# Performance work log

Hardware: AMD Instinct MI355X
Metric: run time of the kernel (lower is better)

The kernel has to match this reference:

```python
import jax, jax.numpy as jnp
import numpy as np

N_NODES = 50000
N_EDGES = 800000
N_GRAPHS = 64
EMB_DIM = 24
N_KERNELS = 2
M_DIM = 64
FOURIER = 4
POS_DIM = 3
EDGE_IN = 2 * FOURIER + 1 + 2 * EMB_DIM  # 57
MLP_DIM = 256
N_OUT = 4
FFNN_IN = EMB_DIM * (N_KERNELS + 1)  # 72


def _lin(key, fan_in, fan_out, stack=None):
    # xavier-uniform weight, zero bias (matches weights_init)
    lim = (6.0 / (fan_in + fan_out)) ** 0.5
    shp = ((stack,) if stack else ()) + (fan_in, fan_out)
    w = jax.random.uniform(key, shp, minval=-lim, maxval=lim, dtype=jnp.float32)
    b = jnp.zeros(((stack,) if stack else ()) + (fan_out,), jnp.float32)
    return w, b


def setup_inputs() -> dict:
    key = jax.random.key(0)
    ks = jax.random.split(key, 20)
    z = jax.random.randint(ks[0], (N_NODES,), 0, 22)
    pos = jax.random.normal(ks[1], (N_NODES, POS_DIM), jnp.float32)
    edge_index = jax.random.randint(ks[2], (2, N_EDGES), 0, N_NODES)
    batch_idx = jnp.sort(jax.random.randint(ks[3], (N_NODES,), 0, N_GRAPHS))
    lim_e = (6.0 / (22 + EMB_DIM)) ** 0.5
    emb_table = jax.random.uniform(ks[4], (22, EMB_DIM), minval=-lim_e, maxval=lim_e, dtype=jnp.float32)
    emb_w, emb_b = _lin(ks[5], EMB_DIM, EMB_DIM)
    # EGNN kernel params, stacked over N_KERNELS
    ew1, eb1 = _lin(ks[6], EDGE_IN, EDGE_IN * 2, N_KERNELS)
    ew2, eb2 = _lin(ks[7], EDGE_IN * 2, M_DIM, N_KERNELS)
    cw1, cb1 = _lin(ks[8], M_DIM, M_DIM * 4, N_KERNELS)
    cw2, cb2 = _lin(ks[9], M_DIM * 4, 1, N_KERNELS)
    nw1, nb1 = _lin(ks[10], EMB_DIM + M_DIM, EMB_DIM * 2, N_KERNELS)
    nw2, nb2 = _lin(ks[11], EMB_DIM * 2, EMB_DIM, N_KERNELS)
    # ffnn: Linear(72,256), Linear(256,256), Linear(256,256), Linear(256,4)
    f0w, f0b = _lin(ks[12], FFNN_IN, MLP_DIM)
    f1w, f1b = _lin(ks[13], MLP_DIM, MLP_DIM)
    f2w, f2b = _lin(ks[14], MLP_DIM, MLP_DIM)
    fow, fob = _lin(ks[15], MLP_DIM, N_OUT)
    return dict(z=z, pos=pos, edge_index=edge_index, batch_idx=batch_idx,
                emb_table=emb_table, emb_w=emb_w, emb_b=emb_b,
                ew1=ew1, eb1=eb1, ew2=ew2, eb2=eb2,
                cw1=cw1, cb1=cb1, cw2=cw2, cb2=cb2,
                nw1=nw1, nb1=nb1, nw2=nw2, nb2=nb2,
                f0w=f0w, f0b=f0b, f1w=f1w, f1b=f1b, f2w=f2w, f2b=f2b,
                fow=fow, fob=fob)


def _egnn_layer(feats, coors, src, dst, ew1, eb1, ew2, eb2, cw1, cb1, cw2, cb2, nw1, nb1, nw2, nb2):
    # EGNN_sparse (PyG flow source_to_target: i=dst=edge_index[1], j=src=edge_index[0])
    rel = coors[src] - coors[dst]                       # [E,3]
    d = jnp.sum(rel * rel, axis=-1, keepdims=True)      # [E,1] squared distance
    scales = 2.0 ** jnp.arange(FOURIER, dtype=feats.dtype)
    ds = d / scales                                     # [E,4]
    edge_feat = jnp.concatenate([jnp.sin(ds), jnp.cos(ds), d], axis=-1)  # [E,9]
    e_in = jnp.concatenate([feats[dst], feats[src], edge_feat], axis=-1)  # [E,57]
    m_ij = jax.nn.silu(jax.nn.silu(e_in @ ew1 + eb1) @ ew2 + eb2)         # [E,64]
    coor_w = jax.nn.silu(m_ij @ cw1 + cb1) @ cw2 + cb2                    # [E,1]
    coors_out = coors + jax.ops.segment_sum(coor_w * rel, dst, num_segments=N_NODES)
    m_i = jax.ops.segment_sum(m_ij, dst, num_segments=N_NODES)            # [N,64]
    h = jax.nn.silu(jnp.concatenate([feats, m_i], axis=-1) @ nw1 + nb1)
    feats_out = feats + (h @ nw2 + nb2)
    return feats_out, coors_out


def reference(z, pos, edge_index, batch_idx, emb_table, emb_w, emb_b,
              ew1, eb1, ew2, eb2, cw1, cb1, cw2, cb2, nw1, nb1, nw2, nb2,
              f0w, f0b, f1w, f1b, f2w, f2b, fow, fob):
    src, dst = edge_index[0], edge_index[1]
    feats = emb_table[z] @ emb_w + emb_b
    coors = pos
    flist = [feats]
    for k in range(N_KERNELS):
        feats, coors = _egnn_layer(feats, coors, src, dst,
                                   ew1[k], eb1[k], ew2[k], eb2[k],
                                   cw1[k], cb1[k], cw2[k], cb2[k],
                                   nw1[k], nb1[k], nw2[k], nb2[k])
        flist.append(feats)
    x = jax.nn.silu(jnp.concatenate(flist, axis=-1))     # [N,72]
    x = jax.nn.silu(x @ f0w + f0b)
    x = jax.nn.silu(x @ f1w + f1b)
    x = jax.nn.silu(x @ f2w + f2b)                       # [N,256]
    cnt = jax.ops.segment_sum(jnp.ones((x.shape[0],), x.dtype), batch_idx, num_segments=N_GRAPHS)
    pooled = jax.ops.segment_sum(x, batch_idx, num_segments=N_GRAPHS) / jnp.maximum(cnt, 1.0)[:, None]
    return jax.nn.sigmoid(pooled @ fow + fob)            # [B,4]
```

## Files before the change

### kernel.cpp

```cpp
#include <hip/hip_runtime.h>
#include <hip/hip_bf16.h>

#define N_NODES  50000
#define N_EDGES  800000
#define N_GRAPHS 64
#define EMB      24
#define MDIM     64
#define EDGE_IN  57
#define EH       114
#define CH       256
#define NIN      88
#define NH       48
#define MLP      256
#define ETILE    128
#define NTILE    64

typedef __bf16 bf16_t;
typedef __bf16 bf16x8 __attribute__((ext_vector_type(8)));
typedef __bf16 bf16x4 __attribute__((ext_vector_type(4)));
typedef float  f32x4  __attribute__((ext_vector_type(4)));

__device__ __forceinline__ float siluf(float x) {
    return x * __builtin_amdgcn_rcpf(1.0f + __expf(-x));
}

__device__ __forceinline__ f32x4 silu4(f32x4 x) {
    f32x4 t = x * (-1.44269504088896341f);
    f32x4 e;
    e[0] = __builtin_amdgcn_exp2f(t[0]);
    e[1] = __builtin_amdgcn_exp2f(t[1]);
    e[2] = __builtin_amdgcn_exp2f(t[2]);
    e[3] = __builtin_amdgcn_exp2f(t[3]);
    f32x4 den = e + 1.0f;
    f32x4 r;
    r[0] = __builtin_amdgcn_rcpf(den[0]);
    r[1] = __builtin_amdgcn_rcpf(den[1]);
    r[2] = __builtin_amdgcn_rcpf(den[2]);
    r[3] = __builtin_amdgcn_rcpf(den[3]);
    return x * r;
}

__device__ __forceinline__ bf16x8 cat44(bf16x4 a, bf16x4 b) {
    bf16x8 r;
    r[0]=a[0]; r[1]=a[1]; r[2]=a[2]; r[3]=a[3];
    r[4]=b[0]; r[5]=b[1]; r[6]=b[2]; r[7]=b[3];
    return r;
}

__global__ void embed_kernel(const int* __restrict__ z, const float* __restrict__ table,
                             const float* __restrict__ w, const float* __restrict__ b,
                             const int* __restrict__ batch, float* __restrict__ f0,
                             bf16_t* __restrict__ fb0, float* __restrict__ cnt)
{
    int n = blockIdx.x * blockDim.x + threadIdx.x;
    if (n >= N_NODES) return;
    float r[EMB];
    const float4* tr = reinterpret_cast<const float4*>(table + z[n] * EMB);
    #pragma unroll
    for (int q = 0; q < 6; q++) {
        float4 v = tr[q];
        r[q*4] = v.x; r[q*4+1] = v.y; r[q*4+2] = v.z; r[q*4+3] = v.w;
    }
    float o[EMB];
    #pragma unroll
    for (int j = 0; j < EMB; j++) o[j] = b[j];
    #pragma unroll
    for (int i = 0; i < EMB; i++) {
        #pragma unroll
        for (int j = 0; j < EMB; j++) o[j] = fmaf(r[i], w[i*EMB + j], o[j]);
    }
    float4* dst = reinterpret_cast<float4*>(f0 + (size_t)n * EMB);
    #pragma unroll
    for (int q = 0; q < 6; q++) dst[q] = make_float4(o[q*4], o[q*4+1], o[q*4+2], o[q*4+3]);
    bf16x8* bdst = reinterpret_cast<bf16x8*>(fb0 + (size_t)n * EMB);
    #pragma unroll
    for (int q = 0; q < 3; q++) {
        bf16x8 pk;
        #pragma unroll
        for (int j = 0; j < 8; j++) pk[j] = (bf16_t)o[q*8 + j];
        bdst[q] = pk;
    }
    atomicAdd(&cnt[batch[n]], 1.0f);
}

#define PK_W1   (128*64)
#define PK_W2   (64*128)
#define PK_CW   (256*64)
#define PK_F0   (256*128)
#define PK_FM   (256*256)
#define PK_TOT  (2*PK_W1 + 2*PK_W2 + PK_CW + PK_F0 + 2*PK_FM)
__global__ void pack_kernel(const float* __restrict__ ew1, const float* __restrict__ eb1,
                            const float* __restrict__ ew2, const float* __restrict__ eb2,
                            const float* __restrict__ cw1, const float* __restrict__ f0w,
                            const float* __restrict__ f1w, const float* __restrict__ f2w,
                            bf16_t* __restrict__ pw)
{
    int idx = blockIdx.x * blockDim.x + threadIdx.x;
    if (idx >= PK_TOT) return;
    float v = 0.0f;
    if (idx < 2 * PK_W1) {
        int l = idx / PK_W1, r = idx - l * PK_W1;
        int n = r >> 6, k = r & 63;
        if (n < EH && k < EDGE_IN)       v = ew1[(l * EDGE_IN + k) * EH + n];
        else if (n < EH && k == EDGE_IN) v = eb1[l * EH + n];
    } else if (idx < 2 * PK_W1 + 2 * PK_W2) {
        int r0 = idx - 2 * PK_W1;
        int l = r0 / PK_W2, r = r0 - l * PK_W2;
        int n = r >> 7, kp = r & 127;
        int ks = kp >> 5, g = (kp >> 3) & 3, j = kp & 7;
        int f = 16 * (2*ks + (j >> 2)) + 4*g + (j & 3);
        if (f < EH)       v = ew2[(l * EH + f) * MDIM + n];
        else if (f == EH) v = eb2[l * MDIM + n];
    } else if (idx < 2 * PK_W1 + 2 * PK_W2 + PK_CW) {
        int r = idx - (2 * PK_W1 + 2 * PK_W2);
        int n = r >> 6, kp = r & 63;
        int ks = kp >> 5, g = (kp >> 3) & 3, j = kp & 7;
        int f = 16 * (2*ks + (j >> 2)) + 4*g + (j & 3);
        v = cw1[f * CH + n];
    } else if (idx < 2 * PK_W1 + 2 * PK_W2 + PK_CW + PK_F0) {
        int r = idx - (2 * PK_W1 + 2 * PK_W2 + PK_CW);
        int n = r >> 7, k = r & 127;
        if (k < 72) v = f0w[k * MLP + n];
    } else {
        int r0 = idx - (2 * PK_W1 + 2 * PK_W2 + PK_CW + PK_F0);
        int l = r0 / PK_FM, r = r0 - l * PK_FM;
        int n = r >> 8, k = r & 255;
        v = (l == 0) ? f1w[k * MLP + n] : f2w[k * MLP + n];
    }
    pw[idx] = (bf16_t)v;
}

__global__ void hist_kernel(const int* __restrict__ dst, int* __restrict__ deg)
{
    int e = blockIdx.x * blockDim.x + threadIdx.x;
    if (e < N_EDGES) atomicAdd(&deg[dst[e]], 1);
}

__global__ __launch_bounds__(1024)
void scan_kernel(const int* __restrict__ deg, int* __restrict__ cursor)
{
    __shared__ int part[1024];
    int t = threadIdx.x;
    const int PER = 49;
    int base = t * PER;
    int s = 0;
    for (int i = 0; i < PER; i++) {
        int p = base + i;
        if (p < N_NODES) s += deg[p];
    }
    part[t] = s;
    __syncthreads();
    for (int off = 1; off < 1024; off <<= 1) {
        int add = (t >= off) ? part[t - off] : 0;
        __syncthreads();
        part[t] += add;
        __syncthreads();
    }
    int run = (t > 0) ? part[t - 1] : 0;
    for (int i = 0; i < PER; i++) {
        int p = base + i;
        if (p < N_NODES) { cursor[p] = run; run += deg[p]; }
    }
}

__global__ void scatter_kernel(const int* __restrict__ src, const int* __restrict__ dst,
                               int* __restrict__ cursor, int* __restrict__ srcs_s,
                               int* __restrict__ dsts_s)
{
    int e = blockIdx.x * blockDim.x + threadIdx.x;
    if (e >= N_EDGES) return;
    int d = dst[e];
    int pos = atomicAdd(&cursor[d], 1);
    srcs_s[pos] = src[e];
    dsts_s[pos] = d;
}

template<int COOR>
__global__ __launch_bounds__(256, 4)
void edge_mfma(const bf16_t* __restrict__ fb, const float* __restrict__ coors,
               const int* __restrict__ srcs_s, const int* __restrict__ dsts_s,
               const bf16_t* __restrict__ W1t, const bf16_t* __restrict__ W2t,
               const bf16_t* __restrict__ CW1t, const float* __restrict__ cb1,
               const float* __restrict__ cw2, const float* __restrict__ cb2,
               float* __restrict__ m_i, float* __restrict__ cdelta)
{
    __shared__ __align__(16) char R1raw[4 * 4096];
    __shared__ float s_rel[COOR ? ETILE * 3 : 4];
    __shared__ float s_cacc[COOR ? ETILE : 4];
    __shared__ int   s_dst[ETILE];

    const int t = threadIdx.x;
    const int w = t >> 6;
    const int l = t & 63;
    const int row0 = w * 32;
    const int ebase = blockIdx.x * ETILE;
    const int l15 = l & 15, l4 = l >> 4;
    bf16_t* slab16 = (bf16_t*)(R1raw + w * 4096);

    {
        int e_loc = t >> 1, half = t & 1;
        int e_l = e_loc & 31;
        int e = ebase + e_loc;
        int s = srcs_s[e], d = dsts_s[e];
        if (half == 0) {
            s_dst[e_loc] = d;
            const bf16x8* fp = reinterpret_cast<const bf16x8*>(fb + (size_t)d * EMB);
            #pragma unroll
            for (int g = 0; g < 3; g++)
                *(bf16x8*)&slab16[e_l*64 + (g ^ (e_l & 7))*8] = fp[g];
        } else {
            const bf16x8* fp = reinterpret_cast<const bf16x8*>(fb + (size_t)s * EMB);
            #pragma unroll
            for (int g = 0; g < 3; g++)
                *(bf16x8*)&slab16[e_l*64 + ((g + 3) ^ (e_l & 7))*8] = fp[g];
            float rx = coors[s*3+0] - coors[d*3+0];
            float ry = coors[s*3+1] - coors[d*3+1];
            float rz = coors[s*3+2] - coors[d*3+2];
            float d2 = rx*rx + ry*ry + rz*rz;
            if (COOR) { s_rel[e_loc*3+0] = rx; s_rel[e_loc*3+1] = ry; s_rel[e_loc*3+2] = rz; }
            bf16x8 p6, p7;
            p6[0]=(bf16_t)__sinf(d2);        p6[1]=(bf16_t)__sinf(d2*0.5f);
            p6[2]=(bf16_t)__sinf(d2*0.25f);  p6[3]=(bf16_t)__sinf(d2*0.125f);
            p6[4]=(bf16_t)__cosf(d2);        p6[5]=(bf16_t)__cosf(d2*0.5f);
            p6[6]=(bf16_t)__cosf(d2*0.25f);  p6[7]=(bf16_t)__cosf(d2*0.125f);
            p7[0]=(bf16_t)d2; p7[1]=(bf16_t)1.0f;
            p7[2]=(bf16_t)0.f; p7[3]=(bf16_t)0.f; p7[4]=(bf16_t)0.f;
            p7[5]=(bf16_t)0.f; p7[6]=(bf16_t)0.f; p7[7]=(bf16_t)0.f;
            *(bf16x8*)&slab16[e_l*64 + (6 ^ (e_l & 7))*8] = p6;
            *(bf16x8*)&slab16[e_l*64 + (7 ^ (e_l & 7))*8] = p7;
        }
    }

    f32x4 acc1[2][8];
    #pragma unroll
    for (int et = 0; et < 2; et++)
        #pragma unroll
        for (int ft = 0; ft < 8; ft++) acc1[et][ft] = (f32x4){0.f,0.f,0.f,0.f};
    __builtin_amdgcn_s_setprio(1);
    #pragma unroll
    for (int ks = 0; ks < 2; ks++) {
        bf16x8 bfrag[2];
        #pragma unroll
        for (int et = 0; et < 2; et++) {
            int e_l = et*16 + l15;
            bfrag[et] = *(const bf16x8*)&slab16[e_l*64 + ((ks*4 + l4) ^ (e_l & 7))*8];
        }
        #pragma unroll
        for (int ft = 0; ft < 8; ft++) {
            bf16x8 a = *(const bf16x8*)&W1t[(ft*16 + l15)*64 + (ks*4 + l4)*8];
            acc1[0][ft] = __builtin_amdgcn_mfma_f32_16x16x32_bf16(a, bfrag[0], acc1[0][ft], 0, 0, 0);
            acc1[1][ft] = __builtin_amdgcn_mfma_f32_16x16x32_bf16(a, bfrag[1], acc1[1][ft], 0, 0, 0);
        }
    }
    __builtin_amdgcn_s_setprio(0);

    bf16x4 h1b[2][8];
    #pragma unroll
    for (int et = 0; et < 2; et++)
        #pragma unroll
        for (int ft = 0; ft < 8; ft++) {
            f32x4 hv = silu4(acc1[et][ft]);
            if (ft == 7 && l4 == 0) hv[2] = 1.0f;
            bf16x4 pk;
            #pragma unroll
            for (int r4 = 0; r4 < 4; r4++) pk[r4] = (bf16_t)hv[r4];
            h1b[et][ft] = pk;
        }

    f32x4 acc2[2][4];
    #pragma unroll
    for (int et = 0; et < 2; et++)
        #pragma unroll
        for (int ft = 0; ft < 4; ft++) acc2[et][ft] = (f32x4){0.f,0.f,0.f,0.f};
    __builtin_amdgcn_s_setprio(1);
    #pragma unroll
    for (int ks = 0; ks < 4; ks++) {
        bf16x8 bfrag0 = cat44(h1b[0][2*ks], h1b[0][2*ks+1]);
        bf16x8 bfrag1 = cat44(h1b[1][2*ks], h1b[1][2*ks+1]);
        #pragma unroll
        for (int ft = 0; ft < 4; ft++) {
            bf16x8 a = *(const bf16x8*)&W2t[(ft*16 + l15)*128 + (ks*4 + l4)*8];
            acc2[0][ft] = __builtin_amdgcn_mfma_f32_16x16x32_bf16(a, bfrag0, acc2[0][ft], 0, 0, 0);
            acc2[1][ft] = __builtin_amdgcn_mfma_f32_16x16x32_bf16(a, bfrag1, acc2[1][ft], 0, 0, 0);
        }
    }
    __builtin_amdgcn_s_setprio(0);

    bf16x4 mb[2][4];
    #pragma unroll
    for (int et = 0; et < 2; et++)
        #pragma unroll
        for (int ft = 0; ft < 4; ft++) {
            int e_l = et*16 + l15;
            int f0 = ft*16 + l4*4;
            f32x4 mv = silu4(acc2[et][ft]);
            bf16x4 pk;
            #pragma unroll
            for (int r4 = 0; r4 < 4; r4++) pk[r4] = (bf16_t)mv[r4];
            mb[et][ft] = pk;
            *(bf16x4*)&slab16[e_l*64 + (((f0 >> 2) ^ (e_l & 7)) << 2)] = pk;
        }

    {
        int col = l;
        int gsw = col >> 2, cw = col & 3;
        int cur = s_dst[row0];
        float run = 0.f;
        for (int i = 0; i < 32; i++) {
            int d = s_dst[row0 + i];
            float v = (float)slab16[i*64 + ((gsw ^ (i & 7)) << 2) + cw];
            if (d != cur) { atomicAdd(&m_i[(size_t)cur*64 + col], run); run = 0.f; cur = d; }
            run += v;
        }
        atomicAdd(&m_i[(size_t)cur*64 + col], run);
    }

    if (COOR) {
        f32x4 csumv0 = (f32x4){0.f,0.f,0.f,0.f};
        f32x4 csumv1 = (f32x4){0.f,0.f,0.f,0.f};
        #pragma unroll
        for (int half = 0; half < 2; half++) {
            f32x4 acc3[2][8];
            #pragma unroll
            for (int et = 0; et < 2; et++)
                #pragma unroll
                for (int ft = 0; ft < 8; ft++) acc3[et][ft] = (f32x4){0.f,0.f,0.f,0.f};
            __builtin_amdgcn_s_setprio(1);
            #pragma unroll
            for (int ks = 0; ks < 2; ks++) {
                bf16x8 bfrag0 = cat44(mb[0][2*ks], mb[0][2*ks+1]);
                bf16x8 bfrag1 = cat44(mb[1][2*ks], mb[1][2*ks+1]);
                #pragma unroll
                for (int ft = 0; ft < 8; ft++) {
                    bf16x8 a = *(const bf16x8*)&CW1t[(half*128 + ft*16 + l15)*64 + (ks*4 + l4)*8];
                    acc3[0][ft] = __builtin_amdgcn_mfma_f32_16x16x32_bf16(a, bfrag0, acc3[0][ft], 0, 0, 0);
                    acc3[1][ft] = __builtin_amdgcn_mfma_f32_16x16x32_bf16(a, bfrag1, acc3[1][ft], 0, 0, 0);
                }
            }
            __builtin_amdgcn_s_setprio(0);
            #pragma unroll
            for (int ft = 0; ft < 8; ft++) {
                int f0 = half*128 + ft*16 + l4*4;
                f32x4 c1 = *(const f32x4*)&cb1[f0];
                f32x4 w2 = *(const f32x4*)&cw2[f0];
                csumv0 += silu4(acc3[0][ft] + c1) * w2;
                csumv1 += silu4(acc3[1][ft] + c1) * w2;
            }
        }
        float csum0 = (csumv0[0] + csumv0[1]) + (csumv0[2] + csumv0[3]);
        float csum1 = (csumv1[0] + csumv1[1]) + (csumv1[2] + csumv1[3]);
        csum0 += __shfl_xor(csum0, 16);
        csum0 += __shfl_xor(csum0, 32);
        csum1 += __shfl_xor(csum1, 16);
        csum1 += __shfl_xor(csum1, 32);
        float cb2v = cb2[0];
        if (l < 32) {
            s_cacc[row0 + l] = ((l & 16) ? csum1 : csum0) + cb2v;
        }
        if (l < 32) {
            int row = row0 + l;
            int d = s_dst[row];
            bool head = (l == 0) || (s_dst[row - 1] != d);
            if (head) {
                float ax = 0.f, ay = 0.f, az = 0.f;
                int i = l;
                do {
                    int r = row0 + i;
                    float c = s_cacc[r];
                    ax = fmaf(c, s_rel[r*3+0], ax);
                    ay = fmaf(c, s_rel[r*3+1], ay);
                    az = fmaf(c, s_rel[r*3+2], az);
                    ++i;
                } while (i < 32 && s_dst[row0 + i] == d);
                atomicAdd(&cdelta[d*3+0], ax);
                atomicAdd(&cdelta[d*3+1], ay);
                atomicAdd(&cdelta[d*3+2], az);
            }
        }
    }
}

template<int EMIT_BF16>
__global__ __launch_bounds__(256)
void node_kernel(const float* __restrict__ feats, const float* __restrict__ m_i,
                 const float* __restrict__ nw1, const float* __restrict__ nb1,
                 const float* __restrict__ nw2, const float* __restrict__ nb2,
                 float* __restrict__ fout, bf16_t* __restrict__ fbout)
{
    __shared__ float s_w1t[NH * NIN];
    __shared__ float s_b1[NH];
    __shared__ float s_w2[NH * EMB];
    __shared__ float s_b2[EMB];
    const int tid = threadIdx.x;
    for (int idx = tid; idx < NH * NIN; idx += 256) {
        int k = idx / NIN, i = idx - k * NIN;
        s_w1t[idx] = nw1[i * NH + k];
    }
    for (int idx = tid; idx < NH * EMB; idx += 256) s_w2[idx] = nw2[idx];
    if (tid < NH) s_b1[tid] = nb1[tid];
    if (tid < EMB) s_b2[tid] = nb2[tid];
    __syncthreads();

    int n = blockIdx.x * 256 + tid;
    if (n >= N_NODES) return;

    float in[NIN];
    const float4* fp = reinterpret_cast<const float4*>(feats + (size_t)n * EMB);
    #pragma unroll
    for (int q = 0; q < 6; q++) {
        float4 v = fp[q];
        in[q*4] = v.x; in[q*4+1] = v.y; in[q*4+2] = v.z; in[q*4+3] = v.w;
    }
    const float4* mp = reinterpret_cast<const float4*>(m_i + (size_t)n * MDIM);
    #pragma unroll
    for (int q = 0; q < 16; q++) {
        float4 v = mp[q];
        in[EMB+q*4] = v.x; in[EMB+q*4+1] = v.y; in[EMB+q*4+2] = v.z; in[EMB+q*4+3] = v.w;
    }
    float o[EMB];
    #pragma unroll
    for (int j = 0; j < EMB; j++) o[j] = in[j] + s_b2[j];
    for (int k = 0; k < NH; k++) {
        const float* w1 = &s_w1t[k * NIN];
        float a0 = 0.f, a1 = 0.f, a2 = 0.f, a3 = 0.f;
        #pragma unroll
        for (int i = 0; i < NIN; i += 4) {
            a0 = fmaf(in[i],   w1[i],   a0);
            a1 = fmaf(in[i+1], w1[i+1], a1);
            a2 = fmaf(in[i+2], w1[i+2], a2);
            a3 = fmaf(in[i+3], w1[i+3], a3);
        }
        float h = siluf(s_b1[k] + ((a0 + a1) + (a2 + a3)));
        const float* w2 = &s_w2[k * EMB];
        #pragma unroll
        for (int j = 0; j < EMB; j++) o[j] = fmaf(h, w2[j], o[j]);
    }
    float4* dst = reinterpret_cast<float4*>(fout + (size_t)n * EMB);
    #pragma unroll
    for (int q = 0; q < 6; q++) dst[q] = make_float4(o[q*4], o[q*4+1], o[q*4+2], o[q*4+3]);
    if (EMIT_BF16) {
        bf16x8* bdst = reinterpret_cast<bf16x8*>(fbout + (size_t)n * EMB);
        #pragma unroll
        for (int q = 0; q < 3; q++) {
            bf16x8 pk;
            #pragma unroll
            for (int j = 0; j < 8; j++) pk[j] = (bf16_t)o[q*8 + j];
            bdst[q] = pk;
        }
    }
}

__global__ void coor_kernel(const float* __restrict__ pos, const float* __restrict__ cdelta,
                            float* __restrict__ out)
{
    int i = blockIdx.x * blockDim.x + threadIdx.x;
    if (i < N_NODES * 3) out[i] = pos[i] + cdelta[i];
}

__global__ __launch_bounds__(512, 4)
void ffnn_fused(const float* __restrict__ f0, const float* __restrict__ f1,
                const float* __restrict__ f2,
                const bf16_t* __restrict__ W0p, const bf16_t* __restrict__ W1p,
                const bf16_t* __restrict__ W2p,
                const float* __restrict__ b0, const float* __restrict__ b1,
                const float* __restrict__ b2,
                const int* __restrict__ batch, float* __restrict__ pooled)
{
    __shared__ __align__(16) bf16_t sH[NTILE * 256];
    __shared__ int s_batch[NTILE];
    const int t = threadIdx.x;
    const int w = t >> 6, l = t & 63;
    const int l15 = l & 15, q = l >> 4;
    const int mt = w & 3;
    const int nh = w >> 2;
    const int mrow0 = mt * 16;
    const int n0 = blockIdx.x * NTILE;

    {
        int row = t >> 3, part = t & 7;
        int n = n0 + row;
        bool valid = n < N_NODES;
        if (part == 7) s_batch[row] = valid ? batch[n] : -1;
        #pragma unroll
        for (int gi = 0; gi < 2; gi++) {
            int g = part * 2 + gi;
            bf16x8 pk;
            #pragma unroll
            for (int j = 0; j < 8; j++) pk[j] = (bf16_t)0.f;
            if (valid && g < 9) {
                const float* sp = (g < 3) ? f0 + (size_t)n*EMB + 8*g
                                : (g < 6) ? f1 + (size_t)n*EMB + 8*(g-3)
                                          : f2 + (size_t)n*EMB + 8*(g-6);
                float4 a = ((const float4*)sp)[0], b = ((const float4*)sp)[1];
                f32x4 sa = silu4((f32x4){a.x, a.y, a.z, a.w});
                f32x4 sb = silu4((f32x4){b.x, b.y, b.z, b.w});
                pk[0]=(bf16_t)sa[0]; pk[1]=(bf16_t)sa[1]; pk[2]=(bf16_t)sa[2]; pk[3]=(bf16_t)sa[3];
                pk[4]=(bf16_t)sb[0]; pk[5]=(bf16_t)sb[1]; pk[6]=(bf16_t)sb[2]; pk[7]=(bf16_t)sb[3];
            }
            *(bf16x8*)&sH[row*128 + (g ^ (row & 7))*8] = pk;
        }
    }
    __syncthreads();

    bf16x8 a0[4];
    {
        int r = mrow0 + l15;
        #pragma unroll
        for (int ks = 0; ks < 4; ks++)
            a0[ks] = *(const bf16x8*)&sH[r*128 + ((ks*4 + q) ^ (r & 7))*8];
    }
    __syncthreads();

    f32x4 acc[8];
    #pragma unroll
    for (int nt = 0; nt < 8; nt++) {
        float bv = b0[(nh*8 + nt)*16 + l15];
        acc[nt] = (f32x4){bv, bv, bv, bv};
    }
    #pragma unroll
    for (int ks = 0; ks < 4; ks++)
        #pragma unroll
        for (int nt = 0; nt < 8; nt++) {
            int n = (nh*8 + nt)*16 + l15;
            bf16x8 b = *(const bf16x8*)&W0p[n*128 + (ks*4 + q)*8];
            acc[nt] = __builtin_amdgcn_mfma_f32_16x16x32_bf16(a0[ks], b, acc[nt], 0, 0, 0);
        }
    #pragma unroll
    for (int nt = 0; nt < 8; nt++) {
        f32x4 sv = silu4(acc[nt]);
        #pragma unroll
        for (int r4 = 0; r4 < 4; r4++) {
            int row = mrow0 + q*4 + r4;
            int col = (nh*8 + nt)*16 + l15;
            sH[row*256 + ((col >> 3) ^ (row & 7))*8 + (col & 7)] = (bf16_t)sv[r4];
        }
    }
    __syncthreads();

    #pragma unroll
    for (int layer = 0; layer < 2; layer++) {
        const bf16_t* Wp = layer ? W2p : W1p;
        const float*  bb = layer ? b2  : b1;
        #pragma unroll
        for (int nt = 0; nt < 8; nt++) {
            float bv = bb[(nh*8 + nt)*16 + l15];
            acc[nt] = (f32x4){bv, bv, bv, bv};
        }
        for (int ks = 0; ks < 8; ks++) {
            int r = mrow0 + l15;
            bf16x8 a = *(const bf16x8*)&sH[r*256 + ((ks*4 + q) ^ (r & 7))*8];
            #pragma unroll
            for (int nt = 0; nt < 8; nt++) {
                int n = (nh*8 + nt)*16 + l15;
                bf16x8 b = *(const bf16x8*)&Wp[n*256 + (ks*4 + q)*8];
                acc[nt] = __builtin_amdgcn_mfma_f32_16x16x32_bf16(a, b, acc[nt], 0, 0, 0);
            }
        }
        __syncthreads();
        #pragma unroll
        for (int nt = 0; nt < 8; nt++) {
            f32x4 sv = silu4(acc[nt]);
            #pragma unroll
            for (int r4 = 0; r4 < 4; r4++) {
                int row = mrow0 + q*4 + r4;
                int col = (nh*8 + nt)*16 + l15;
                sH[row*256 + ((col >> 3) ^ (row & 7))*8 + (col & 7)] = (bf16_t)sv[r4];
            }
        }
        __syncthreads();
    }

    {
        int j = t & 255;
        int rh = t >> 8;
        int g = j >> 3, jo = j & 7;
        int cur = -1;
        float run = 0.f;
        for (int i = rh*32; i < rh*32 + 32; i++) {
            int bb = s_batch[i];
            if (bb != cur) {
                if (cur >= 0) atomicAdd(&pooled[cur * MLP + j], run);
                run = 0.f; cur = bb;
            }
            if (bb >= 0) run += (float)sH[i*256 + (g ^ (i & 7))*8 + jo];
        }
        if (cur >= 0) atomicAdd(&pooled[cur * MLP + j], run);
    }
}

__global__ void final_kernel(const float* __restrict__ pooled, const float* __restrict__ cnt,
                             const float* __restrict__ fow, const float* __restrict__ fob,
                             float* __restrict__ out)
{
    int t = threadIdx.x;
    int bg = t >> 2, o = t & 3;
    float c = fmaxf(cnt[bg], 1.0f);
    float acc = 0.f;
    for (int i = 0; i < MLP; i++) acc = fmaf(pooled[bg * MLP + i], fow[i * 4 + o], acc);
    acc = acc / c + fob[o];
    out[t] = 1.0f / (1.0f + __expf(-acc));
}

extern "C" void kernel_launch(void* const* d_in, const int* in_sizes, int n_in,
                              void* d_out, int out_size, void* d_ws, size_t ws_size,
                              hipStream_t stream)
{
    const int*   z     = (const int*)  d_in[0];
    const float* pos   = (const float*)d_in[1];
    const int*   eidx  = (const int*)  d_in[2];
    const int*   batch = (const int*)  d_in[3];
    const float* embt  = (const float*)d_in[4];
    const float* embw  = (const float*)d_in[5];
    const float* embb  = (const float*)d_in[6];
    const float* ew1   = (const float*)d_in[7];
    const float* eb1   = (const float*)d_in[8];
    const float* ew2   = (const float*)d_in[9];
    const float* eb2   = (const float*)d_in[10];
    const float* cw1   = (const float*)d_in[11];
    const float* cb1   = (const float*)d_in[12];
    const float* cw2   = (const float*)d_in[13];
    const float* cb2   = (const float*)d_in[14];
    const float* nw1   = (const float*)d_in[15];
    const float* nb1   = (const float*)d_in[16];
    const float* nw2   = (const float*)d_in[17];
    const float* nb2   = (const float*)d_in[18];
    const float* f0w   = (const float*)d_in[19];
    const float* f0b   = (const float*)d_in[20];
    const float* f1w   = (const float*)d_in[21];
    const float* f1b   = (const float*)d_in[22];
    const float* f2w   = (const float*)d_in[23];
    const float* f2b   = (const float*)d_in[24];
    const float* fow   = (const float*)d_in[25];
    const float* fob   = (const float*)d_in[26];

    float* ws     = (float*)d_ws;
    float* f0     = ws;
    float* f1v    = f0 + (size_t)N_NODES * EMB;
    float* f2v    = f1v + (size_t)N_NODES * EMB;
    bf16_t* fb0   = (bf16_t*)(f2v + (size_t)N_NODES * EMB);
    bf16_t* fb1   = fb0 + (size_t)N_NODES * EMB;
    float* coorsA = (float*)(fb1 + (size_t)N_NODES * EMB);
    float* cdelta = coorsA + N_NODES * 3;
    float* m_i    = cdelta + N_NODES * 3;
    float* pooled = m_i + (size_t)N_NODES * MDIM;
    float* cnt    = pooled + N_GRAPHS * MLP;
    int*   deg    = (int*)(cnt + N_GRAPHS);
    int*   cursor = deg + N_NODES;
    int*   srcs_s = cursor + N_NODES;
    int*   dsts_s = srcs_s + N_EDGES;
    bf16_t* packw = (bf16_t*)(dsts_s + N_EDGES);
    bf16_t* W1t0  = packw;
    bf16_t* W1t1  = W1t0 + PK_W1;
    bf16_t* W2t0  = W1t1 + PK_W1;
    bf16_t* W2t1  = W2t0 + PK_W2;
    bf16_t* CW1t  = W2t1 + PK_W2;
    bf16_t* W0p   = CW1t + PK_CW;
    bf16_t* W1p   = W0p + PK_F0;
    bf16_t* W2p   = W1p + PK_FM;

    hipMemsetAsync(cdelta, 0, N_NODES * 3 * sizeof(float), stream);
    hipMemsetAsync(m_i, 0, (size_t)N_NODES * MDIM * sizeof(float), stream);
    hipMemsetAsync(pooled, 0, (N_GRAPHS * MLP + N_GRAPHS) * sizeof(float), stream);
    hipMemsetAsync(deg, 0, N_NODES * sizeof(int), stream);

    const int* e_src = eidx;
    const int* e_dst = eidx + N_EDGES;
    pack_kernel<<<(PK_TOT + 255) / 256, 256, 0, stream>>>(ew1, eb1, ew2, eb2, cw1,
                                                          f0w, f1w, f2w, packw);
    hist_kernel<<<(N_EDGES + 255) / 256, 256, 0, stream>>>(e_dst, deg);
    scan_kernel<<<1, 1024, 0, stream>>>(deg, cursor);
    scatter_kernel<<<(N_EDGES + 255) / 256, 256, 0, stream>>>(e_src, e_dst, cursor, srcs_s, dsts_s);

    embed_kernel<<<(N_NODES + 255) / 256, 256, 0, stream>>>(z, embt, embw, embb, batch, f0, fb0, cnt);

    const int EBLK = N_EDGES / ETILE;
    edge_mfma<1><<<EBLK, 256, 0, stream>>>(fb0, pos, srcs_s, dsts_s,
        W1t0, W2t0, CW1t, cb1, cw2, cb2, m_i, cdelta);
    node_kernel<1><<<(N_NODES + 255) / 256, 256, 0, stream>>>(f0, m_i, nw1, nb1, nw2, nb2, f1v, fb1);
    coor_kernel<<<(N_NODES * 3 + 255) / 256, 256, 0, stream>>>(pos, cdelta, coorsA);
    hipMemsetAsync(m_i, 0, (size_t)N_NODES * MDIM * sizeof(float), stream);
    edge_mfma<0><<<EBLK, 256, 0, stream>>>(fb1, coorsA, srcs_s, dsts_s,
        W1t1, W2t1, CW1t, cb1, cw2, cb2, m_i, nullptr);
    node_kernel<0><<<(N_NODES + 255) / 256, 256, 0, stream>>>(f1v, m_i,
        nw1 + NIN * NH, nb1 + NH, nw2 + NH * EMB, nb2 + EMB, f2v, nullptr);

    const int FBLK = (N_NODES + NTILE - 1) / NTILE;
    ffnn_fused<<<FBLK, 512, 0, stream>>>(f0, f1v, f2v, W0p, W1p, W2p,
                                         f0b, f1b, f2b, batch, pooled);

    final_kernel<<<1, 256, 0, stream>>>(pooled, cnt, fow, fob, (float*)d_out);
}
```

Baseline: 971.6 us.

## Process two edge tiles per block, gathering both before computing

The edge kernel is split into gather and compute helpers, and each block now handles two 128-edge tiles. Both tiles' gathers are issued up front so their global memory latency overlaps, then the MLP/MFMA compute runs on each tile in turn. Shared memory per block doubles, which may reduce occupancy, and the grid is halved.

New measurement: 1.494 ms. +53.8%, slower.

```diff
diff --git a/kernel.cpp b/kernel.cpp
--- a/kernel.cpp
+++ b/kernel.cpp
@@ -176,60 +176,58 @@
 }
 
 template<int COOR>
-__global__ __launch_bounds__(256, 4)
-void edge_mfma(const bf16_t* __restrict__ fb, const float* __restrict__ coors,
-               const int* __restrict__ srcs_s, const int* __restrict__ dsts_s,
-               const bf16_t* __restrict__ W1t, const bf16_t* __restrict__ W2t,
-               const bf16_t* __restrict__ CW1t, const float* __restrict__ cb1,
-               const float* __restrict__ cw2, const float* __restrict__ cb2,
-               float* __restrict__ m_i, float* __restrict__ cdelta)
-{
-    __shared__ __align__(16) char R1raw[4 * 4096];
-    __shared__ float s_rel[COOR ? ETILE * 3 : 4];
-    __shared__ float s_cacc[COOR ? ETILE : 4];
-    __shared__ int   s_dst[ETILE];
-
-    const int t = threadIdx.x;
-    const int w = t >> 6;
-    const int l = t & 63;
+__device__ __forceinline__ void edge_gather(
+    const bf16_t* __restrict__ fb, const float* __restrict__ coors,
+    const int* __restrict__ srcs_s, const int* __restrict__ dsts_s,
+    int ebase, int t, bf16_t* __restrict__ slab,
+    float* __restrict__ s_rel, int* __restrict__ s_dst)
+{
+    int e_loc = t >> 1, half = t & 1;
+    int e_l = e_loc & 31;
+    int e = ebase + e_loc;
+    int s = srcs_s[e], d = dsts_s[e];
+    if (half == 0) {
+        s_dst[e_loc] = d;
+        const bf16x8* fp = reinterpret_cast<const bf16x8*>(fb + (size_t)d * EMB);
+        #pragma unroll
+        for (int g = 0; g < 3; g++)
+            *(bf16x8*)&slab[e_l*64 + (g ^ (e_l & 7))*8] = fp[g];
+    } else {
+        const bf16x8* fp = reinterpret_cast<const bf16x8*>(fb + (size_t)s * EMB);
+        #pragma unroll
+        for (int g = 0; g < 3; g++)
+            *(bf16x8*)&slab[e_l*64 + ((g + 3) ^ (e_l & 7))*8] = fp[g];
+        float rx = coors[s*3+0] - coors[d*3+0];
+        float ry = coors[s*3+1] - coors[d*3+1];
+        float rz = coors[s*3+2] - coors[d*3+2];
+        float d2 = rx*rx + ry*ry + rz*rz;
+        if (COOR) { s_rel[e_loc*3+0] = rx; s_rel[e_loc*3+1] = ry; s_rel[e_loc*3+2] = rz; }
+        bf16x8 p6, p7;
+        p6[0]=(bf16_t)__sinf(d2);        p6[1]=(bf16_t)__sinf(d2*0.5f);
+        p6[2]=(bf16_t)__sinf(d2*0.25f);  p6[3]=(bf16_t)__sinf(d2*0.125f);
+        p6[4]=(bf16_t)__cosf(d2);        p6[5]=(bf16_t)__cosf(d2*0.5f);
+        p6[6]=(bf16_t)__cosf(d2*0.25f);  p6[7]=(bf16_t)__cosf(d2*0.125f);
+        p7[0]=(bf16_t)d2; p7[1]=(bf16_t)1.0f;
+        p7[2]=(bf16_t)0.f; p7[3]=(bf16_t)0.f; p7[4]=(bf16_t)0.f;
+        p7[5]=(bf16_t)0.f; p7[6]=(bf16_t)0.f; p7[7]=(bf16_t)0.f;
+        *(bf16x8*)&slab[e_l*64 + (6 ^ (e_l & 7))*8] = p6;
+        *(bf16x8*)&slab[e_l*64 + (7 ^ (e_l & 7))*8] = p7;
+    }
+}
+
+template<int COOR>
+__device__ __forceinline__ void edge_compute(
+    const bf16_t* __restrict__ W1t, const bf16_t* __restrict__ W2t,
+    const bf16_t* __restrict__ CW1t, const float* __restrict__ cb1,
+    const float* __restrict__ cw2, const float* __restrict__ cb2,
+    float* __restrict__ m_i, float* __restrict__ cdelta,
+    int t, bf16_t* __restrict__ slab,
+    const float* __restrict__ s_rel, float* __restrict__ s_cacc,
+    const int* __restrict__ s_dst)
+{
+    const int w = t >> 6, l = t & 63;
     const int row0 = w * 32;
-    const int ebase = blockIdx.x * ETILE;
     const int l15 = l & 15, l4 = l >> 4;
-    bf16_t* slab16 = (bf16_t*)(R1raw + w * 4096);
-
-    {
-        int e_loc = t >> 1, half = t & 1;
-        int e_l = e_loc & 31;
-        int e = ebase + e_loc;
-        int s = srcs_s[e], d = dsts_s[e];
-        if (half == 0) {
-            s_dst[e_loc] = d;
-            const bf16x8* fp = reinterpret_cast<const bf16x8*>(fb + (size_t)d * EMB);
-            #pragma unroll
-            for (int g = 0; g < 3; g++)
-                *(bf16x8*)&slab16[e_l*64 + (g ^ (e_l & 7))*8] = fp[g];
-        } else {
-            const bf16x8* fp = reinterpret_cast<const bf16x8*>(fb + (size_t)s * EMB);
-            #pragma unroll
-            for (int g = 0; g < 3; g++)
-                *(bf16x8*)&slab16[e_l*64 + ((g + 3) ^ (e_l & 7))*8] = fp[g];
-            float rx = coors[s*3+0] - coors[d*3+0];
-            float ry = coors[s*3+1] - coors[d*3+1];
-            float rz = coors[s*3+2] - coors[d*3+2];
-            float d2 = rx*rx + ry*ry + rz*rz;
-            if (COOR) { s_rel[e_loc*3+0] = rx; s_rel[e_loc*3+1] = ry; s_rel[e_loc*3+2] = rz; }
-            bf16x8 p6, p7;
-            p6[0]=(bf16_t)__sinf(d2);        p6[1]=(bf16_t)__sinf(d2*0.5f);
-            p6[2]=(bf16_t)__sinf(d2*0.25f);  p6[3]=(bf16_t)__sinf(d2*0.125f);
-            p6[4]=(bf16_t)__cosf(d2);        p6[5]=(bf16_t)__cosf(d2*0.5f);
-            p6[6]=(bf16_t)__cosf(d2*0.25f);  p6[7]=(bf16_t)__cosf(d2*0.125f);
-            p7[0]=(bf16_t)d2; p7[1]=(bf16_t)1.0f;
-            p7[2]=(bf16_t)0.f; p7[3]=(bf16_t)0.f; p7[4]=(bf16_t)0.f;
-            p7[5]=(bf16_t)0.f; p7[6]=(bf16_t)0.f; p7[7]=(bf16_t)0.f;
-            *(bf16x8*)&slab16[e_l*64 + (6 ^ (e_l & 7))*8] = p6;
-            *(bf16x8*)&slab16[e_l*64 + (7 ^ (e_l & 7))*8] = p7;
-        }
-    }
 
     f32x4 acc1[2][8];
     #pragma unroll
@@ -243,7 +241,7 @@
         #pragma unroll
         for (int et = 0; et < 2; et++) {
             int e_l = et*16 + l15;
-            bfrag[et] = *(const bf16x8*)&slab16[e_l*64 + ((ks*4 + l4) ^ (e_l & 7))*8];
+            bfrag[et] = *(const bf16x8*)&slab[e_l*64 + ((ks*4 + l4) ^ (e_l & 7))*8];
         }
         #pragma unroll
         for (int ft = 0; ft < 8; ft++) {
@@ -297,8 +295,8 @@
             bf16x4 pk;
             #pragma unroll
             for (int r4 = 0; r4 < 4; r4++) pk[r4] = (bf16_t)mv[r4];
-            mb[et][ft] = pk;
-            *(bf16x4*)&slab16[e_l*64 + (((f0 >> 2) ^ (e_l & 7)) << 2)] = pk;
+            if (COOR) mb[et][ft] = pk;
+            *(bf16x4*)&slab[e_l*64 + (((f0 >> 2) ^ (e_l & 7)) << 2)] = pk;
         }
 
     {
@@ -308,7 +306,7 @@
         float run = 0.f;
         for (int i = 0; i < 32; i++) {
             int d = s_dst[row0 + i];
-            float v = (float)slab16[i*64 + ((gsw ^ (i & 7)) << 2) + cw];
+            float v = (float)slab[i*64 + ((gsw ^ (i & 7)) << 2) + cw];
             if (d != cur) { atomicAdd(&m_i[(size_t)cur*64 + col], run); run = 0.f; cur = d; }
             run += v;
         }
@@ -378,6 +376,38 @@
             }
         }
     }
+}
+
+template<int COOR>
+__global__ __launch_bounds__(256, 4)
+void edge_mfma(const bf16_t* __restrict__ fb, const float* __restrict__ coors,
+               const int* __restrict__ srcs_s, const int* __restrict__ dsts_s,
+               const bf16_t* __restrict__ W1t, const bf16_t* __restrict__ W2t,
+               const bf16_t* __restrict__ CW1t, const float* __restrict__ cb1,
+               const float* __restrict__ cw2, const float* __restrict__ cb2,
+               float* __restrict__ m_i, float* __restrict__ cdelta)
+{
+    __shared__ __align__(16) char R1raw[4 * 8192];
+    __shared__ float s_rel[COOR ? 2*ETILE*3 : 4];
+    __shared__ float s_cacc[COOR ? 2*ETILE : 4];
+    __shared__ int   s_dst[2*ETILE];
+
+    const int t = threadIdx.x;
+    const int w = t >> 6;
+    const int ebase = blockIdx.x * (2*ETILE);
+
+    bf16_t* slabA = (bf16_t*)(R1raw + w*8192);
+    bf16_t* slabB = (bf16_t*)(R1raw + w*8192 + 4096);
+    const int ro = COOR ? ETILE*3 : 0;
+    const int co = COOR ? ETILE : 0;
+
+    edge_gather<COOR>(fb, coors, srcs_s, dsts_s, ebase,         t, slabA, s_rel,      s_dst);
+    edge_gather<COOR>(fb, coors, srcs_s, dsts_s, ebase + ETILE, t, slabB, s_rel + ro, s_dst + ETILE);
+
+    edge_compute<COOR>(W1t, W2t, CW1t, cb1, cw2, cb2, m_i, cdelta,
+                       t, slabA, s_rel,      s_cacc,      s_dst);
+    edge_compute<COOR>(W1t, W2t, CW1t, cb1, cw2, cb2, m_i, cdelta,
+                       t, slabB, s_rel + ro, s_cacc + co, s_dst + ETILE);
 }
 
 template<int EMIT_BF16>
@@ -673,7 +703,7 @@
 
     embed_kernel<<<(N_NODES + 255) / 256, 256, 0, stream>>>(z, embt, embw, embb, batch, f0, fb0, cnt);
 
-    const int EBLK = N_EDGES / ETILE;
+    const int EBLK = N_EDGES / (2 * ETILE);
     edge_mfma<1><<<EBLK, 256, 0, stream>>>(fb0, pos, srcs_s, dsts_s,
         W1t0, W2t0, CW1t, cb1, cw2, cb2, m_i, cdelta);
     node_kernel<1><<<(N_NODES + 255) / 256, 256, 0, stream>>>(f0, m_i, nw1, nb1, nw2, nb2, f1v, fb1);
```
